# Optimization experiments

Measured on AMD Instinct MI355X. Metric: run time of the kernel, lower is better.

## Reference

```python
import jax, jax.numpy as jnp
import numpy as np

N, M, OBS_LEN, PRED_LEN = 8192, 32, 8, 12
H, E = 128, 64
RADIUS = 2.0


def _lstm_cell(x, h, c, Wih, Whh, bih, bhh):
    # torch LSTMCell gate order: i, f, g, o
    g = x @ Wih + h @ Whh + bih + bhh
    i, f, gg, o = jnp.split(g, 4, axis=-1)
    c_new = jax.nn.sigmoid(f) * c + jax.nn.sigmoid(i) * jnp.tanh(gg)
    h_new = jax.nn.sigmoid(o) * jnp.tanh(c_new)
    return h_new, c_new


def _social_pool(focal_pos, nb_pos, nb_h, nb_mask, pW, pb, sW, sb):
    rel = nb_pos - focal_pos[:, None, :]                    # (N,M,2)
    dist = jnp.sqrt(jnp.sum(rel * rel, axis=-1))            # (N,M)
    valid = (dist <= RADIUS) & nb_mask                      # (N,M) bool
    pos_feat = jax.nn.relu(rel @ pW + pb)                   # (N,M,E)
    comb = jnp.concatenate([nb_h, pos_feat], axis=-1)       # (N,M,H+E)
    pooled = jax.nn.relu(comb @ sW + sb) * valid[..., None] # (N,M,H)
    social = pooled.max(axis=1) * valid.any(axis=1, keepdims=True)
    return social                                            # (N,H)


def setup_inputs() -> dict:
    key = jax.random.key(0)
    ks = jax.random.split(key, 12)
    def w(k, shape, fan_in):
        return (jax.random.normal(k, shape, jnp.float32) / np.float32(np.sqrt(fan_in)))
    return {
        'obs': jax.random.normal(ks[0], (N, OBS_LEN, 2), jnp.float32),
        'nb_obs': jax.random.normal(ks[1], (N, M, OBS_LEN, 2), jnp.float32),
        'nb_mask': jax.random.randint(ks[2], (N, M), 0, 2) > 0,
        'we_enc_W': w(ks[3], (2, E), 2), 'we_enc_b': jnp.zeros((E,), jnp.float32),
        'enc_Wih': w(ks[4], (E, 4 * H), E), 'enc_Whh': w(ks[5], (H, 4 * H), H),
        'enc_bih': jnp.zeros((4 * H,), jnp.float32), 'enc_bhh': jnp.zeros((4 * H,), jnp.float32),
        'sp_pos_W': w(ks[6], (2, E), 2), 'sp_pos_b': jnp.zeros((E,), jnp.float32),
        'sp_soc_W': w(ks[7], (H + E, H), H + E), 'sp_soc_b': jnp.zeros((H,), jnp.float32),
        'we_dec_W': w(ks[8], (2, E), 2), 'we_dec_b': jnp.zeros((E,), jnp.float32),
        'dec_Wih': w(ks[9], (E + H, 4 * H), E + H), 'dec_Whh': w(ks[10], (H, 4 * H), H),
        'dec_bih': jnp.zeros((4 * H,), jnp.float32), 'dec_bhh': jnp.zeros((4 * H,), jnp.float32),
        'out_W': w(ks[11], (H, 5), H), 'out_b': jnp.zeros((5,), jnp.float32),
    }


def reference(obs, nb_obs, nb_mask,
              we_enc_W, we_enc_b, enc_Wih, enc_Whh, enc_bih, enc_bhh,
              sp_pos_W, sp_pos_b, sp_soc_W, sp_soc_b,
              we_dec_W, we_dec_b, dec_Wih, dec_Whh, dec_bih, dec_bhh,
              out_W, out_b):
    n = obs.shape[0]
    origin = obs[:, -1:, :]                       # (N,1,2)
    obs_rel = obs - origin                        # (N,T,2)
    nb_rel = nb_obs - nb_obs[:, :, -1:, :]        # (N,M,T,2) (inputs contain no NaN)

    h0 = jnp.zeros((n, H), obs.dtype)
    c0 = jnp.zeros((n, H), obs.dtype)

    def enc_step(carry, xs):
        h, c = carry
        focal, nb_pos = xs                        # (N,2), (N,M,2)
        nb_h = jnp.broadcast_to(h[:, None, :], (n, M, H))
        social = _social_pool(focal, nb_pos, nb_h, nb_mask, sp_pos_W, sp_pos_b, sp_soc_W, sp_soc_b)
        emb = jax.nn.relu(focal @ we_enc_W + we_enc_b)
        h, c = _lstm_cell(emb, h, c, enc_Wih, enc_Whh, enc_bih, enc_bhh)
        h = h + 0.3 * social
        return (h, c), None

    xs = (jnp.swapaxes(obs_rel, 0, 1), jnp.moveaxis(nb_rel, 2, 0))
    (h, c), _ = jax.lax.scan(enc_step, (h0, c0), xs)

    nb_pos_last = jnp.zeros((n, M, 2), obs.dtype)
    nb_h_last = jnp.broadcast_to(h[:, None, :], (n, M, H))  # frozen encoder h
    cur0 = jnp.zeros((n, 2), obs.dtype)

    def dec_step(carry, _):
        h, c, cur = carry
        social = _social_pool(cur, nb_pos_last, nb_h_last, nb_mask, sp_pos_W, sp_pos_b, sp_soc_W, sp_soc_b)
        emb = jax.nn.relu(cur @ we_dec_W + we_dec_b)
        inp = jnp.concatenate([emb, social], axis=-1)
        h, c = _lstm_cell(inp, h, c, dec_Wih, dec_Whh, dec_bih, dec_bhh)
        raw = h @ out_W + out_b                   # dropout = identity (eval)
        mu = raw[:, :2]
        sigma = jnp.exp(jnp.clip(raw[:, 2:4], -4.0, 4.0))
        rho = jnp.tanh(raw[:, 4:5])
        return (h, c, mu), (mu, sigma, rho)

    _, (mus, sigmas, rhos) = jax.lax.scan(dec_step, (h, c, cur0), None, length=PRED_LEN)
    mus = jnp.swapaxes(mus, 0, 1) + origin        # (N,pred_len,2)
    sigmas = jnp.swapaxes(sigmas, 0, 1)           # (N,pred_len,2)
    rhos = jnp.swapaxes(rhos, 0, 1)               # (N,pred_len,1)
    return mus, sigmas, rhos
```

## Files before the change

kernel.cpp:

```cpp
#include <hip/hip_runtime.h>
#include <math.h>

typedef short bf16x8 __attribute__((ext_vector_type(8)));
typedef float f32x4  __attribute__((ext_vector_type(4)));

#define N_AG 8192
#define GA   16
#define BLK  512
#define TOB  8
#define TPR  12

#define PK_ENC 0
#define PK_DEC 98304
#define PK_WB  262144
#define PK_WT  270336
#define PK_OUT 286720
#define PK_TOT 288768

__device__ __forceinline__ unsigned short f2bf(float f) {
    unsigned u = __float_as_uint(f);
    return (unsigned short)((u + 0x7FFFu + ((u >> 16) & 1u)) >> 16);
}
__device__ __forceinline__ float bf2f(unsigned short s) {
    return __uint_as_float(((unsigned)s) << 16);
}
__device__ __forceinline__ float v_exp2(float x) {
    float r; asm("v_exp_f32 %0, %1" : "=v"(r) : "v"(x)); return r;
}
__device__ __forceinline__ float v_rcp(float x) {
    float r; asm("v_rcp_f32 %0, %1" : "=v"(r) : "v"(x)); return r;
}
__device__ __forceinline__ unsigned cvtpk(float lo, float hi) {
    unsigned r; asm("v_cvt_pk_bf16_f32 %0, %1, %2" : "=v"(r) : "v"(lo), "v"(hi)); return r;
}
__device__ __forceinline__ float sigm(float x) {
    return v_rcp(1.f + v_exp2(-1.44269504f * x));
}
__device__ __forceinline__ float tanhp(float x) {
    x = fminf(fmaxf(x, -15.f), 15.f);
    float t = v_exp2(2.88539008f * x);
    return 1.f - 2.f * v_rcp(t + 1.f);
}

__global__ void pack_w(const float* __restrict__ eWih, const float* __restrict__ eWhh,
                       const float* __restrict__ dWih, const float* __restrict__ dWhh,
                       const float* __restrict__ sW, const float* __restrict__ oW,
                       unsigned short* __restrict__ pk)
{
    for (int idx = blockIdx.x * blockDim.x + threadIdx.x; idx < PK_TOT;
         idx += gridDim.x * blockDim.x) {
        float v;
        if (idx < PK_DEC) {
            int ks = idx >> 14, rem = idx & 16383;
            int nt = rem >> 9, l = (rem >> 3) & 63, i = rem & 7;
            int klo = ((l >> 4) << 3) + i;
            int col = (nt >> 3) * 128 + (nt & 7) * 16 + (l & 15);
            v = (ks < 2) ? eWih[(ks * 32 + klo) * 512 + col]
                         : eWhh[((ks - 2) * 32 + klo) * 512 + col];
        } else if (idx < PK_WB) {
            int t = idx - PK_DEC;
            int ks = t >> 14, rem = t & 16383;
            int nt = rem >> 9, l = (rem >> 3) & 63, i = rem & 7;
            int klo = ((l >> 4) << 3) + i;
            int col = (nt >> 3) * 128 + (nt & 7) * 16 + (l & 15);
            if (ks < 2)      v = dWih[(ks * 32 + klo) * 512 + col];
            else if (ks < 6) v = dWih[(64 + (ks - 2) * 32 + klo) * 512 + col];
            else             v = dWhh[((ks - 6) * 32 + klo) * 512 + col];
        } else if (idx < PK_WT) {
            int t = idx - PK_WB;
            int ks = t >> 12, rem = t & 4095;
            int nt = rem >> 9, l = (rem >> 3) & 63, i = rem & 7;
            int klo = ((l >> 4) << 3) + i;
            v = sW[(128 + ks * 32 + klo) * 128 + nt * 16 + (l & 15)];
        } else if (idx < PK_OUT) {
            int t = idx - PK_WT;
            int ks = t >> 12, rem = t & 4095;
            int nt = rem >> 9, l = (rem >> 3) & 63, i = rem & 7;
            int klo = ((l >> 4) << 3) + i;
            v = sW[(ks * 32 + klo) * 128 + nt * 16 + (l & 15)];
        } else {
            int t = idx - PK_OUT;
            int ks = t >> 9, r = t & 511;
            int l = r >> 3, i = r & 7;
            int klo = ((l >> 4) << 3) + i;
            int col = l & 15;
            v = (col < 5) ? oW[(ks * 32 + klo) * 5 + col] : 0.f;
        }
        pk[idx] = f2bf(v);
    }
}

__global__ __launch_bounds__(BLK, 4)
void slstm(const float* __restrict__ obs, const float* __restrict__ nb_obs,
           const void* __restrict__ nb_mask,
           const float* __restrict__ weW, const float* __restrict__ web,
           const float* __restrict__ eBih, const float* __restrict__ eBhh,
           const float* __restrict__ pW, const float* __restrict__ pb,
           const float* __restrict__ sb,
           const float* __restrict__ wdW, const float* __restrict__ wdb,
           const float* __restrict__ dBih, const float* __restrict__ dBhh,
           const float* __restrict__ outB,
           const unsigned short* __restrict__ pk,
           float* __restrict__ out)
{
    __shared__ __align__(16) float obsrel[TOB][GA][2];
    __shared__ float origin[GA][2];
    __shared__ __align__(16) float nblast[GA][32][2];
    __shared__ __align__(16) float rel2[GA][32][2];
    __shared__ unsigned vmaskAll[TOB][GA];
    __shared__ int maskb[GA];
    __shared__ int detf;
    __shared__ __align__(16) short hbf[2][GA * 128];
    __shared__ __align__(16) short embb[GA * 64];
    __shared__ __align__(16) short socb[GA * 128];
    __shared__ __align__(16) short pftA[128 * 64];
    __shared__ __align__(16) short pftB[128 * 64];
    __shared__ float cur[GA][2];

    const int j    = threadIdx.x;
    const int lane = j & 63;
    const int w    = j >> 6;
    const int q    = lane >> 4;
    const int r16  = lane & 15;
    const int swz  = (r16 & 7) << 4;
    const int n0   = blockIdx.x * GA;

    if (j < GA) maskb[j] = 0;
    if (j == 0) detf = 0;
    __syncthreads();
    {
        const unsigned* mw = (const unsigned*)nb_mask;
        unsigned w0 = mw[j], w1 = mw[BLK + j];
        int f = 0;
        if (w0 > 1u || w1 > 1u) f |= 1;
        if ((w0 != 0u && w0 != 0x3F800000u) || (w1 != 0u && w1 != 0x3F800000u)) f |= 2;
        if (f) atomicOr(&detf, f);
    }
    __syncthreads();
    const int det = detf;
    {
        int a = j >> 5, i2 = j & 31, gi = (n0 + a) * 32 + i2;
        int bit;
        if (!(det & 1))      bit = ((const int*)nb_mask)[gi] != 0;
        else if (!(det & 2)) bit = (((const float*)nb_mask)[gi] != 0.f);
        else                 bit = ((const unsigned char*)nb_mask)[gi] != 0;
        if (bit) atomicOr(&maskb[a], 1 << i2);
    }
    if (j < 128) {
        int t = j >> 4, a = j & 15;
        float o0 = obs[(n0 + a) * 16 + 14], o1 = obs[(n0 + a) * 16 + 15];
        obsrel[t][a][0] = obs[(n0 + a) * 16 + t * 2]     - o0;
        obsrel[t][a][1] = obs[(n0 + a) * 16 + t * 2 + 1] - o1;
        if (t == 0) { origin[a][0] = o0; origin[a][1] = o1; }
    }
    {
        int a = j >> 5, i2 = j & 31;
        const float* nb = nb_obs + ((size_t)((n0 + a) * 32 + i2)) * 16 + 14;
        nblast[a][i2][0] = nb[0];
        nblast[a][i2][1] = nb[1];
    }
    ((int4*)hbf)[j] = make_int4(0, 0, 0, 0);

    const int e2 = (j & 31) * 2;
    const float pca0 = pW[e2],      pca1 = pW[e2 + 1];
    const float pcc0 = pW[64 + e2], pcc1 = pW[64 + e2 + 1];
    const float pcb0 = pb[e2],      pcb1 = pb[e2 + 1];
    const float ew0 = weW[lane], ew1 = weW[64 + lane], ebv = web[lane];
    const float sbv = sb[w * 16 + r16];
    float bG[4];
    #pragma unroll
    for (int g = 0; g < 4; ++g) {
        int col = g * 128 + w * 16 + r16;
        bG[g] = eBih[col] + eBhh[col];
    }
    const bf16x8* pkE = (const bf16x8*)(pk + PK_ENC);
    const bf16x8* pkD = (const bf16x8*)(pk + PK_DEC);
    const bf16x8* pkB = (const bf16x8*)(pk + PK_WB);
    const bf16x8* pkT = (const bf16x8*)(pk + PK_WT);
    const bf16x8* pkO = (const bf16x8*)(pk + PK_OUT);
    bf16x8 wbf[2];
    #pragma unroll
    for (int ks = 0; ks < 2; ++ks)
        wbf[ks] = pkB[(ks * 8 + w) * 64 + lane];

    float cst[4];
    #pragma unroll
    for (int rg = 0; rg < 4; ++rg) cst[rg] = 0.f;

    const f32x4 zz4 = {0.f, 0.f, 0.f, 0.f};
    int pp = 0;
    __syncthreads();

    {
        int a = j >> 5, i2 = j & 31;
        const float* base = nb_obs + ((size_t)((n0 + a) * 32 + i2)) * 16;
        float nlx = nblast[a][i2][0], nly = nblast[a][i2][1];
        int mbit = (maskb[a] >> i2) & 1;
        #pragma unroll
        for (int t = 0; t < TOB; ++t) {
            float rx = base[2 * t]     - nlx - obsrel[t][a][0];
            float ry = base[2 * t + 1] - nly - obsrel[t][a][1];
            bool ok = (rx * rx + ry * ry <= 4.f) && mbit;
            unsigned long long b = __ballot(ok);
            if ((lane & 31) == 0) vmaskAll[t][2 * w + (lane >> 5)] = (unsigned)(b >> (lane & 32));
            if (t == 0) { rel2[a][i2][0] = rx; rel2[a][i2][1] = ry; }
        }
    }
    {
        float x0 = fmaxf(obsrel[0][w][0] * ew0 + obsrel[0][w][1] * ew1 + ebv, 0.f);
        float x1 = fmaxf(obsrel[0][w + 8][0] * ew0 + obsrel[0][w + 8][1] * ew1 + ebv, 0.f);
        unsigned u = cvtpk(x0, x1);
        char* eb = (char*)embb + w * 128 + ((lane * 2) ^ ((w & 7) << 4));
        *(short*)eb = (short)u;
        *(short*)(eb + 1024) = (short)(u >> 16);
    }
    __syncthreads();

    auto FILL = [&](int c, short* buf) {
        const int half16 = (c >> 1) << 4;
        const int alo = (c & 1) << 3;
        const int rw = j >> 5;
        unsigned woff = (unsigned)(rw * 128 + ((e2 * 2) ^ ((rw & 7) << 4)));
        const float* rptr = &rel2[alo][half16 + rw][0];
        #pragma unroll
        for (int s = 0; s < 8; ++s) {
            float rx = rptr[0], ry = rptr[1];
            float v0 = fmaxf(fmaf(ry, pcc0, fmaf(rx, pca0, pcb0)), 0.f);
            float v1 = fmaxf(fmaf(ry, pcc1, fmaf(rx, pca1, pcb1)), 0.f);
            *(unsigned*)((char*)buf + woff) = cvtpk(v0, v1);
            woff += 2048;
            rptr += 64;
        }
    };
    auto SOCIAL = [&](int c, const short* buf, float* ms, int t) {
        const int half16 = (c >> 1) << 4;
        const int alo = (c & 1) << 3;
        __builtin_amdgcn_s_setprio(1);
        #pragma unroll 4
        for (int aLoc = 0; aLoc < 8; ++aLoc) {
            int a = alo + aLoc;
            const char* pb2 = (const char*)buf + (aLoc * 16 + r16) * 128;
            bf16x8 af0 = *(const bf16x8*)(pb2 + ((q * 16) ^ swz));
            bf16x8 af1 = *(const bf16x8*)(pb2 + ((64 + q * 16) ^ swz));
            f32x4 ac = __builtin_amdgcn_mfma_f32_16x16x32_bf16(af0, wbf[0], zz4, 0, 0, 0);
            ac = __builtin_amdgcn_mfma_f32_16x16x32_bf16(af1, wbf[1], ac, 0, 0, 0);
            unsigned vbs = vmaskAll[t][a] >> (half16 + q * 4);
            float pm = ((vbs >> 0) & 1) ? ac[0] : -3e38f;
            pm = fmaxf(pm, ((vbs >> 1) & 1) ? ac[1] : -3e38f);
            pm = fmaxf(pm, ((vbs >> 2) & 1) ? ac[2] : -3e38f);
            pm = fmaxf(pm, ((vbs >> 3) & 1) ? ac[3] : -3e38f);
            pm = fmaxf(pm, __shfl_xor(pm, 16));
            pm = fmaxf(pm, __shfl_xor(pm, 32));
            if (q == (a >> 2)) ms[a & 3] = fmaxf(ms[a & 3], pm);
        }
        __builtin_amdgcn_s_setprio(0);
    };

    #pragma unroll 1
    for (int t = 0; t < TOB; ++t) {
        float ms[4];
        #pragma unroll
        for (int rg = 0; rg < 4; ++rg) ms[rg] = -3e38f;
        f32x4 hpA = zz4;
        f32x4 ag[4];
        #pragma unroll
        for (int g = 0; g < 4; ++g) ag[g] = zz4;
        const short* hb = hbf[pp];
        short* hw = hbf[pp ^ 1];

        FILL(0, pftA);
        __builtin_amdgcn_s_setprio(1);
        #pragma unroll
        for (int ks = 0; ks < 4; ++ks) {
            bf16x8 af = *(const bf16x8*)((const char*)hb + r16 * 256 +
                          (((ks * 32 + q * 8) * 2) ^ swz));
            bf16x8 bfr = pkT[(ks * 8 + w) * 64 + lane];
            hpA = __builtin_amdgcn_mfma_f32_16x16x32_bf16(af, bfr, hpA, 0, 0, 0);
        }
        #pragma unroll 2
        for (int ks = 0; ks < 6; ++ks) {
            bf16x8 af = (ks < 2)
                ? *(const bf16x8*)((const char*)embb + r16 * 128 +
                      (((ks * 32 + q * 8) * 2) ^ swz))
                : *(const bf16x8*)((const char*)hb + r16 * 256 +
                      ((((ks - 2) * 32 + q * 8) * 2) ^ swz));
            #pragma unroll
            for (int g = 0; g < 4; ++g) {
                bf16x8 bfr = pkE[(ks * 32 + g * 8 + w) * 64 + lane];
                ag[g] = __builtin_amdgcn_mfma_f32_16x16x32_bf16(af, bfr, ag[g], 0, 0, 0);
            }
        }
        __builtin_amdgcn_s_setprio(0);
        __syncthreads();

        FILL(1, pftB);
        SOCIAL(0, pftA, ms, t);
        __syncthreads();

        FILL(2, pftA);
        SOCIAL(1, pftB, ms, t);
        __syncthreads();

        FILL(3, pftB);
        SOCIAL(2, pftA, ms, t);
        __syncthreads();

        SOCIAL(3, pftB, ms, t);
        {
            float hn[4];
            #pragma unroll
            for (int rg = 0; rg < 4; ++rg) {
                float gi = sigm(ag[0][rg] + bG[0]);
                float gf = sigm(ag[1][rg] + bG[1]);
                float gg = tanhp(ag[2][rg] + bG[2]);
                float go = sigm(ag[3][rg] + bG[3]);
                cst[rg] = gf * cst[rg] + gi * gg;
                hn[rg] = go * tanhp(cst[rg]) + 0.3f * fmaxf(ms[rg] + hpA[rg] + sbv, 0.f);
            }
            unsigned u01 = cvtpk(hn[0], hn[1]);
            unsigned u23 = cvtpk(hn[2], hn[3]);
            int hx2 = (w * 16 + r16) * 2;
            *(short*)((char*)hw + (q * 4 + 0) * 256 + (hx2 ^ (((q * 4 + 0) & 7) << 4))) = (short)u01;
            *(short*)((char*)hw + (q * 4 + 1) * 256 + (hx2 ^ (((q * 4 + 1) & 7) << 4))) = (short)(u01 >> 16);
            *(short*)((char*)hw + (q * 4 + 2) * 256 + (hx2 ^ (((q * 4 + 2) & 7) << 4))) = (short)u23;
            *(short*)((char*)hw + (q * 4 + 3) * 256 + (hx2 ^ (((q * 4 + 3) & 7) << 4))) = (short)(u23 >> 16);
        }
        if (t < TOB - 1) {
            int a = j >> 5, i2 = j & 31;
            const float* base = nb_obs + ((size_t)((n0 + a) * 32 + i2)) * 16 + (t + 1) * 2;
            rel2[a][i2][0] = base[0] - nblast[a][i2][0] - obsrel[t + 1][a][0];
            rel2[a][i2][1] = base[1] - nblast[a][i2][1] - obsrel[t + 1][a][1];
            float x0 = fmaxf(obsrel[t + 1][w][0] * ew0 + obsrel[t + 1][w][1] * ew1 + ebv, 0.f);
            float x1 = fmaxf(obsrel[t + 1][w + 8][0] * ew0 + obsrel[t + 1][w + 8][1] * ew1 + ebv, 0.f);
            unsigned u = cvtpk(x0, x1);
            char* eb = (char*)embb + w * 128 + ((lane * 2) ^ ((w & 7) << 4));
            *(short*)eb = (short)u;
            *(short*)(eb + 1024) = (short)(u >> 16);
        }
        __syncthreads();
        pp ^= 1;
    }

    f32x4 hpE = zz4;
    {
        const short* hb = hbf[pp];
        #pragma unroll
        for (int ks = 0; ks < 4; ++ks) {
            bf16x8 af = *(const bf16x8*)((const char*)hb + r16 * 256 +
                          (((ks * 32 + q * 8) * 2) ^ swz));
            bf16x8 bfr = pkT[(ks * 8 + w) * 64 + lane];
            hpE = __builtin_amdgcn_mfma_f32_16x16x32_bf16(af, bfr, hpE, 0, 0, 0);
        }
    }
    #pragma unroll
    for (int g = 0; g < 4; ++g) {
        int col = g * 128 + w * 16 + r16;
        bG[g] = dBih[col] + dBhh[col];
    }
    if (j < 32) cur[j >> 1][j & 1] = 0.f;
    const float obv = outB[r16 < 5 ? r16 : 4];
    __syncthreads();

    #pragma unroll 1
    for (int st = 0; st < TPR; ++st) {
        const short* hb = hbf[pp];
        short* hw = hbf[pp ^ 1];

        bf16x8 embf[2];
        {
            const float cx = cur[r16][0], cy = cur[r16][1];
            f32x4 sa = zz4;
            #pragma unroll
            for (int ks = 0; ks < 2; ++ks) {
                const int e0 = ks * 32 + q * 8;
                float4 a0 = *(const float4*)(pW + e0);
                float4 a1 = *(const float4*)(pW + e0 + 4);
                float4 c0 = *(const float4*)(pW + 64 + e0);
                float4 c1 = *(const float4*)(pW + 64 + e0 + 4);
                float4 b0 = *(const float4*)(pb + e0);
                float4 b1 = *(const float4*)(pb + e0 + 4);
                union { unsigned u[4]; bf16x8 v; } pf;
                pf.u[0] = cvtpk(fmaxf(b0.x - cx * a0.x - cy * c0.x, 0.f),
                                fmaxf(b0.y - cx * a0.y - cy * c0.y, 0.f));
                pf.u[1] = cvtpk(fmaxf(b0.z - cx * a0.z - cy * c0.z, 0.f),
                                fmaxf(b0.w - cx * a0.w - cy * c0.w, 0.f));
                pf.u[2] = cvtpk(fmaxf(b1.x - cx * a1.x - cy * c1.x, 0.f),
                                fmaxf(b1.y - cx * a1.y - cy * c1.y, 0.f));
                pf.u[3] = cvtpk(fmaxf(b1.z - cx * a1.z - cy * c1.z, 0.f),
                                fmaxf(b1.w - cx * a1.w - cy * c1.w, 0.f));
                sa = __builtin_amdgcn_mfma_f32_16x16x32_bf16(pf.v, wbf[ks], sa, 0, 0, 0);
                float4 d0 = *(const float4*)(wdW + e0);
                float4 d1 = *(const float4*)(wdW + e0 + 4);
                float4 g0 = *(const float4*)(wdW + 64 + e0);
                float4 g1 = *(const float4*)(wdW + 64 + e0 + 4);
                float4 h0 = *(const float4*)(wdb + e0);
                float4 h1 = *(const float4*)(wdb + e0 + 4);
                union { unsigned u[4]; bf16x8 v; } em;
                em.u[0] = cvtpk(fmaxf(cx * d0.x + cy * g0.x + h0.x, 0.f),
                                fmaxf(cx * d0.y + cy * g0.y + h0.y, 0.f));
                em.u[1] = cvtpk(fmaxf(cx * d0.z + cy * g0.z + h0.z, 0.f),
                                fmaxf(cx * d0.w + cy * g0.w + h0.w, 0.f));
                em.u[2] = cvtpk(fmaxf(cx * d1.x + cy * g1.x + h1.x, 0.f),
                                fmaxf(cx * d1.y + cy * g1.y + h1.y, 0.f));
                em.u[3] = cvtpk(fmaxf(cx * d1.z + cy * g1.z + h1.z, 0.f),
                                fmaxf(cx * d1.w + cy * g1.w + h1.w, 0.f));
                embf[ks] = em.v;
            }
            float sv[4];
            #pragma unroll
            for (int rg = 0; rg < 4; ++rg) {
                int a = q * 4 + rg;
                float ax = cur[a][0], ay = cur[a][1];
                bool vd = (ax * ax + ay * ay <= 4.f) && (maskb[a] != 0);
                float z = sa[rg] + hpE[rg] + sbv;
                sv[rg] = vd ? fmaxf(z, 0.f) : 0.f;
            }
            unsigned u01 = cvtpk(sv[0], sv[1]);
            unsigned u23 = cvtpk(sv[2], sv[3]);
            int hx2 = (w * 16 + r16) * 2;
            *(short*)((char*)socb + (q * 4 + 0) * 256 + (hx2 ^ (((q * 4 + 0) & 7) << 4))) = (short)u01;
            *(short*)((char*)socb + (q * 4 + 1) * 256 + (hx2 ^ (((q * 4 + 1) & 7) << 4))) = (short)(u01 >> 16);
            *(short*)((char*)socb + (q * 4 + 2) * 256 + (hx2 ^ (((q * 4 + 2) & 7) << 4))) = (short)u23;
            *(short*)((char*)socb + (q * 4 + 3) * 256 + (hx2 ^ (((q * 4 + 3) & 7) << 4))) = (short)(u23 >> 16);
        }
        __syncthreads();

        f32x4 ag[4];
        #pragma unroll
        for (int g = 0; g < 4; ++g) ag[g] = zz4;
        __builtin_amdgcn_s_setprio(1);
        #pragma unroll 2
        for (int ks = 0; ks < 10; ++ks) {
            bf16x8 af;
            if (ks < 2)
                af = embf[ks];
            else if (ks < 6)
                af = *(const bf16x8*)((const char*)socb + r16 * 256 +
                       ((((ks - 2) * 32 + q * 8) * 2) ^ swz));
            else
                af = *(const bf16x8*)((const char*)hb + r16 * 256 +
                       ((((ks - 6) * 32 + q * 8) * 2) ^ swz));
            #pragma unroll
            for (int g = 0; g < 4; ++g) {
                bf16x8 bfr = pkD[(ks * 32 + g * 8 + w) * 64 + lane];
                ag[g] = __builtin_amdgcn_mfma_f32_16x16x32_bf16(af, bfr, ag[g], 0, 0, 0);
            }
        }
        __builtin_amdgcn_s_setprio(0);
        {
            float hn[4];
            #pragma unroll
            for (int rg = 0; rg < 4; ++rg) {
                float gi = sigm(ag[0][rg] + bG[0]);
                float gf = sigm(ag[1][rg] + bG[1]);
                float gg = tanhp(ag[2][rg] + bG[2]);
                float go = sigm(ag[3][rg] + bG[3]);
                cst[rg] = gf * cst[rg] + gi * gg;
                hn[rg] = go * tanhp(cst[rg]);
            }
            unsigned u01 = cvtpk(hn[0], hn[1]);
            unsigned u23 = cvtpk(hn[2], hn[3]);
            int hx2 = (w * 16 + r16) * 2;
            *(short*)((char*)hw + (q * 4 + 0) * 256 + (hx2 ^ (((q * 4 + 0) & 7) << 4))) = (short)u01;
            *(short*)((char*)hw + (q * 4 + 1) * 256 + (hx2 ^ (((q * 4 + 1) & 7) << 4))) = (short)(u01 >> 16);
            *(short*)((char*)hw + (q * 4 + 2) * 256 + (hx2 ^ (((q * 4 + 2) & 7) << 4))) = (short)u23;
            *(short*)((char*)hw + (q * 4 + 3) * 256 + (hx2 ^ (((q * 4 + 3) & 7) << 4))) = (short)(u23 >> 16);
        }
        __syncthreads();
        pp ^= 1;

        {
            const short* hn = hbf[pp];
            f32x4 oc = zz4;
            #pragma unroll
            for (int ks = 0; ks < 4; ++ks) {
                bf16x8 af = *(const bf16x8*)((const char*)hn + r16 * 256 +
                              (((ks * 32 + q * 8) * 2) ^ swz));
                bf16x8 bfr = pkO[ks * 64 + lane];
                oc = __builtin_amdgcn_mfma_f32_16x16x32_bf16(af, bfr, oc, 0, 0, 0);
            }
            if (w == 0 && r16 < 5) {
                #pragma unroll
                for (int rg = 0; rg < 4; ++rg) {
                    int a = q * 4 + rg, n = n0 + a;
                    float r = oc[rg] + obv;
                    if (r16 < 2) {
                        cur[a][r16] = r;
                        out[n * 24 + st * 2 + r16] = r + origin[a][r16];
                    } else if (r16 < 4) {
                        float cl = fminf(fmaxf(r, -4.f), 4.f);
                        out[196608 + n * 24 + st * 2 + (r16 - 2)] = v_exp2(cl * 1.44269504f);
                    } else {
                        out[393216 + n * 12 + st] = tanhp(r);
                    }
                }
            }
        }
        __syncthreads();
    }
}

extern "C" void kernel_launch(void* const* d_in, const int* in_sizes, int n_in,
                              void* d_out, int out_size, void* d_ws, size_t ws_size,
                              hipStream_t stream) {
    const float* obs    = (const float*)d_in[0];
    const float* nb_obs = (const float*)d_in[1];
    const void*  nb_mask= d_in[2];
    const float* weW    = (const float*)d_in[3];
    const float* web    = (const float*)d_in[4];
    const float* encWih = (const float*)d_in[5];
    const float* encWhh = (const float*)d_in[6];
    const float* encBih = (const float*)d_in[7];
    const float* encBhh = (const float*)d_in[8];
    const float* pW     = (const float*)d_in[9];
    const float* pb     = (const float*)d_in[10];
    const float* sW     = (const float*)d_in[11];
    const float* sbv    = (const float*)d_in[12];
    const float* wdW    = (const float*)d_in[13];
    const float* wdb    = (const float*)d_in[14];
    const float* decWih = (const float*)d_in[15];
    const float* decWhh = (const float*)d_in[16];
    const float* decBih = (const float*)d_in[17];
    const float* decBhh = (const float*)d_in[18];
    const float* outW   = (const float*)d_in[19];
    const float* outB   = (const float*)d_in[20];
    float* out = (float*)d_out;
    unsigned short* pkw = (unsigned short*)d_ws;

    pack_w<<<(PK_TOT + 255) / 256, 256, 0, stream>>>(encWih, encWhh, decWih, decWhh, sW, outW, pkw);
    slstm<<<N_AG / GA, BLK, 0, stream>>>(obs, nb_obs, nb_mask, weW, web,
        encBih, encBhh, pW, pb, sbv, wdW, wdb, decBih, decBhh, outB, pkw, out);
}
```

Measured before the change: 318.0 us.

## Recompute decoder output projection redundantly per wave to drop cur LDS and barrier

The output head MFMA now runs at the start of each decoder step in every wave, reading the previous h. The current position is broadcast through lane shuffles instead of a shared cur array, which removes one __syncthreads per step and the LDS round trip. The decoder-embedding computation also moves into the gate MFMA loop so it interleaves with the matrix ops. In exchange, all eight waves repeat the small output projection, and a final epilogue writes the last step's outputs.

```diff
diff --git a/kernel.cpp b/kernel.cpp
--- a/kernel.cpp
+++ b/kernel.cpp
@@ -115,7 +115,6 @@
     __shared__ __align__(16) short socb[GA * 128];
     __shared__ __align__(16) short pftA[128 * 64];
     __shared__ __align__(16) short pftB[128 * 64];
-    __shared__ float cur[GA][2];
 
     const int j    = threadIdx.x;
     const int lane = j & 63;
@@ -357,7 +356,7 @@
         int col = g * 128 + w * 16 + r16;
         bG[g] = dBih[col] + dBhh[col];
     }
-    if (j < 32) cur[j >> 1][j & 1] = 0.f;
+    const float ob0 = outB[0], ob1 = outB[1];
     const float obv = outB[r16 < 5 ? r16 : 4];
     __syncthreads();
 
@@ -366,9 +365,50 @@
         const short* hb = hbf[pp];
         short* hw = hbf[pp ^ 1];
 
-        bf16x8 embf[2];
+        float cx_r = 0.f, cy_r = 0.f;
+        float cxv[4], cyv[4];
+        #pragma unroll
+        for (int rg = 0; rg < 4; ++rg) { cxv[rg] = 0.f; cyv[rg] = 0.f; }
+        if (st > 0) {
+            f32x4 oc = zz4;
+            #pragma unroll
+            for (int ks = 0; ks < 4; ++ks) {
+                bf16x8 af = *(const bf16x8*)((const char*)hb + r16 * 256 +
+                              (((ks * 32 + q * 8) * 2) ^ swz));
+                oc = __builtin_amdgcn_mfma_f32_16x16x32_bf16(af, pkO[ks * 64 + lane], oc, 0, 0, 0);
+            }
+            if (w == 0 && r16 < 5) {
+                #pragma unroll
+                for (int rg = 0; rg < 4; ++rg) {
+                    int a = q * 4 + rg, n = n0 + a;
+                    float r = oc[rg] + obv;
+                    if (r16 < 2) {
+                        out[n * 24 + (st - 1) * 2 + r16] = r + origin[a][r16];
+                    } else if (r16 < 4) {
+                        float cl = fminf(fmaxf(r, -4.f), 4.f);
+                        out[196608 + n * 24 + (st - 1) * 2 + (r16 - 2)] = v_exp2(cl * 1.44269504f);
+                    } else {
+                        out[393216 + n * 12 + (st - 1)] = tanhp(r);
+                    }
+                }
+            }
+            #pragma unroll
+            for (int rg = 0; rg < 4; ++rg) {
+                cxv[rg] = __shfl(oc[rg], (q << 4))     + ob0;
+                cyv[rg] = __shfl(oc[rg], (q << 4) + 1) + ob1;
+            }
+            int srcA = (r16 >> 2) << 4;
+            float s0 = __shfl(oc[0], srcA), s1 = __shfl(oc[1], srcA);
+            float s2 = __shfl(oc[2], srcA), s3 = __shfl(oc[3], srcA);
+            float t0 = __shfl(oc[0], srcA + 1), t1 = __shfl(oc[1], srcA + 1);
+            float t2 = __shfl(oc[2], srcA + 1), t3 = __shfl(oc[3], srcA + 1);
+            int rsel = r16 & 3;
+            float mx0 = (rsel & 1) ? s1 : s0, mx1 = (rsel & 1) ? s3 : s2;
+            float my0 = (rsel & 1) ? t1 : t0, my1 = (rsel & 1) ? t3 : t2;
+            cx_r = ((rsel & 2) ? mx1 : mx0) + ob0;
+            cy_r = ((rsel & 2) ? my1 : my0) + ob1;
+        }
         {
-            const float cx = cur[r16][0], cy = cur[r16][1];
             f32x4 sa = zz4;
             #pragma unroll
             for (int ks = 0; ks < 2; ++ks) {
@@ -380,38 +420,21 @@
                 float4 b0 = *(const float4*)(pb + e0);
                 float4 b1 = *(const float4*)(pb + e0 + 4);
                 union { unsigned u[4]; bf16x8 v; } pf;
-                pf.u[0] = cvtpk(fmaxf(b0.x - cx * a0.x - cy * c0.x, 0.f),
-                                fmaxf(b0.y - cx * a0.y - cy * c0.y, 0.f));
-                pf.u[1] = cvtpk(fmaxf(b0.z - cx * a0.z - cy * c0.z, 0.f),
-                                fmaxf(b0.w - cx * a0.w - cy * c0.w, 0.f));
-                pf.u[2] = cvtpk(fmaxf(b1.x - cx * a1.x - cy * c1.x, 0.f),
-                                fmaxf(b1.y - cx * a1.y - cy * c1.y, 0.f));
-                pf.u[3] = cvtpk(fmaxf(b1.z - cx * a1.z - cy * c1.z, 0.f),
-                                fmaxf(b1.w - cx * a1.w - cy * c1.w, 0.f));
+                pf.u[0] = cvtpk(fmaxf(b0.x - cx_r * a0.x - cy_r * c0.x, 0.f),
+                                fmaxf(b0.y - cx_r * a0.y - cy_r * c0.y, 0.f));
+                pf.u[1] = cvtpk(fmaxf(b0.z - cx_r * a0.z - cy_r * c0.z, 0.f),
+                                fmaxf(b0.w - cx_r * a0.w - cy_r * c0.w, 0.f));
+                pf.u[2] = cvtpk(fmaxf(b1.x - cx_r * a1.x - cy_r * c1.x, 0.f),
+                                fmaxf(b1.y - cx_r * a1.y - cy_r * c1.y, 0.f));
+                pf.u[3] = cvtpk(fmaxf(b1.z - cx_r * a1.z - cy_r * c1.z, 0.f),
+                                fmaxf(b1.w - cx_r * a1.w - cy_r * c1.w, 0.f));
                 sa = __builtin_amdgcn_mfma_f32_16x16x32_bf16(pf.v, wbf[ks], sa, 0, 0, 0);
-                float4 d0 = *(const float4*)(wdW + e0);
-                float4 d1 = *(const float4*)(wdW + e0 + 4);
-                float4 g0 = *(const float4*)(wdW + 64 + e0);
-                float4 g1 = *(const float4*)(wdW + 64 + e0 + 4);
-                float4 h0 = *(const float4*)(wdb + e0);
-                float4 h1 = *(const float4*)(wdb + e0 + 4);
-                union { unsigned u[4]; bf16x8 v; } em;
-                em.u[0] = cvtpk(fmaxf(cx * d0.x + cy * g0.x + h0.x, 0.f),
-                                fmaxf(cx * d0.y + cy * g0.y + h0.y, 0.f));
-                em.u[1] = cvtpk(fmaxf(cx * d0.z + cy * g0.z + h0.z, 0.f),
-                                fmaxf(cx * d0.w + cy * g0.w + h0.w, 0.f));
-                em.u[2] = cvtpk(fmaxf(cx * d1.x + cy * g1.x + h1.x, 0.f),
-                                fmaxf(cx * d1.y + cy * g1.y + h1.y, 0.f));
-                em.u[3] = cvtpk(fmaxf(cx * d1.z + cy * g1.z + h1.z, 0.f),
-                                fmaxf(cx * d1.w + cy * g1.w + h1.w, 0.f));
-                embf[ks] = em.v;
             }
             float sv[4];
             #pragma unroll
             for (int rg = 0; rg < 4; ++rg) {
                 int a = q * 4 + rg;
-                float ax = cur[a][0], ay = cur[a][1];
-                bool vd = (ax * ax + ay * ay <= 4.f) && (maskb[a] != 0);
+                bool vd = (cxv[rg] * cxv[rg] + cyv[rg] * cyv[rg] <= 4.f) && (maskb[a] != 0);
                 float z = sa[rg] + hpE[rg] + sbv;
                 sv[rg] = vd ? fmaxf(z, 0.f) : 0.f;
             }
@@ -429,12 +452,34 @@
         #pragma unroll
         for (int g = 0; g < 4; ++g) ag[g] = zz4;
         __builtin_amdgcn_s_setprio(1);
+        #pragma unroll
+        for (int ks = 0; ks < 2; ++ks) {
+            const int e0 = ks * 32 + q * 8;
+            float4 d0 = *(const float4*)(wdW + e0);
+            float4 d1 = *(const float4*)(wdW + e0 + 4);
+            float4 g0 = *(const float4*)(wdW + 64 + e0);
+            float4 g1 = *(const float4*)(wdW + 64 + e0 + 4);
+            float4 h0 = *(const float4*)(wdb + e0);
+            float4 h1 = *(const float4*)(wdb + e0 + 4);
+            union { unsigned u[4]; bf16x8 v; } em;
+            em.u[0] = cvtpk(fmaxf(cx_r * d0.x + cy_r * g0.x + h0.x, 0.f),
+                            fmaxf(cx_r * d0.y + cy_r * g0.y + h0.y, 0.f));
+            em.u[1] = cvtpk(fmaxf(cx_r * d0.z + cy_r * g0.z + h0.z, 0.f),
+                            fmaxf(cx_r * d0.w + cy_r * g0.w + h0.w, 0.f));
+            em.u[2] = cvtpk(fmaxf(cx_r * d1.x + cy_r * g1.x + h1.x, 0.f),
+                            fmaxf(cx_r * d1.y + cy_r * g1.y + h1.y, 0.f));
+            em.u[3] = cvtpk(fmaxf(cx_r * d1.z + cy_r * g1.z + h1.z, 0.f),
+                            fmaxf(cx_r * d1.w + cy_r * g1.w + h1.w, 0.f));
+            #pragma unroll
+            for (int g = 0; g < 4; ++g) {
+                bf16x8 bfr = pkD[(ks * 32 + g * 8 + w) * 64 + lane];
+                ag[g] = __builtin_amdgcn_mfma_f32_16x16x32_bf16(em.v, bfr, ag[g], 0, 0, 0);
+            }
+        }
         #pragma unroll 2
-        for (int ks = 0; ks < 10; ++ks) {
+        for (int ks = 2; ks < 10; ++ks) {
             bf16x8 af;
-            if (ks < 2)
-                af = embf[ks];
-            else if (ks < 6)
+            if (ks < 6)
                 af = *(const bf16x8*)((const char*)socb + r16 * 256 +
                        ((((ks - 2) * 32 + q * 8) * 2) ^ swz));
             else
@@ -468,35 +513,32 @@
         }
         __syncthreads();
         pp ^= 1;
-
-        {
-            const short* hn = hbf[pp];
-            f32x4 oc = zz4;
-            #pragma unroll
-            for (int ks = 0; ks < 4; ++ks) {
-                bf16x8 af = *(const bf16x8*)((const char*)hn + r16 * 256 +
-                              (((ks * 32 + q * 8) * 2) ^ swz));
-                bf16x8 bfr = pkO[ks * 64 + lane];
-                oc = __builtin_amdgcn_mfma_f32_16x16x32_bf16(af, bfr, oc, 0, 0, 0);
-            }
-            if (w == 0 && r16 < 5) {
-                #pragma unroll
-                for (int rg = 0; rg < 4; ++rg) {
-                    int a = q * 4 + rg, n = n0 + a;
-                    float r = oc[rg] + obv;
-                    if (r16 < 2) {
-                        cur[a][r16] = r;
-                        out[n * 24 + st * 2 + r16] = r + origin[a][r16];
-                    } else if (r16 < 4) {
-                        float cl = fminf(fmaxf(r, -4.f), 4.f);
-                        out[196608 + n * 24 + st * 2 + (r16 - 2)] = v_exp2(cl * 1.44269504f);
-                    } else {
-                        out[393216 + n * 12 + st] = tanhp(r);
-                    }
+    }
+
+    if (w == 0) {
+        const short* hb = hbf[pp];
+        f32x4 oc = zz4;
+        #pragma unroll
+        for (int ks = 0; ks < 4; ++ks) {
+            bf16x8 af = *(const bf16x8*)((const char*)hb + r16 * 256 +
+                          (((ks * 32 + q * 8) * 2) ^ swz));
+            oc = __builtin_amdgcn_mfma_f32_16x16x32_bf16(af, pkO[ks * 64 + lane], oc, 0, 0, 0);
+        }
+        if (r16 < 5) {
+            #pragma unroll
+            for (int rg = 0; rg < 4; ++rg) {
+                int a = q * 4 + rg, n = n0 + a;
+                float r = oc[rg] + obv;
+                if (r16 < 2) {
+                    out[n * 24 + (TPR - 1) * 2 + r16] = r + origin[a][r16];
+                } else if (r16 < 4) {
+                    float cl = fminf(fmaxf(r, -4.f), 4.f);
+                    out[196608 + n * 24 + (TPR - 1) * 2 + (r16 - 2)] = v_exp2(cl * 1.44269504f);
+                } else {
+                    out[393216 + n * 12 + (TPR - 1)] = tanhp(r);
                 }
             }
         }
-        __syncthreads();
     }
 }
 
```

Result: faster. 308.9 us (-2.9%).
